# Performance work log

Measured on AMD Instinct MI355X. Metric: run time of the kernel, lower is better.

## Reference

```python
import jax, jax.numpy as jnp
import numpy as np

S = 2048       # seq_len
D = 1024       # d_model
H = 16         # heads
DK = 64        # d_k = d_v = D // H


def setup_inputs() -> dict:
    key = jax.random.key(0)
    ks = jax.random.split(key, 12)
    sc_in = 1.0 / np.sqrt(D)
    return {
        "Q": jax.random.normal(ks[0], (S, D), jnp.float32),
        "K": jax.random.normal(ks[1], (S, D), jnp.float32),
        "V": jax.random.normal(ks[2], (S, D), jnp.float32),
        # stacked per-head projection weights (torch Linear math: x @ W + b, W stored [in,out])
        "Wq": jax.random.normal(ks[3], (H, D, DK), jnp.float32) * sc_in,
        "bq": jnp.zeros((H, DK), jnp.float32),
        "Wk": jax.random.normal(ks[4], (H, D, DK), jnp.float32) * sc_in,
        "bk": jnp.zeros((H, DK), jnp.float32),
        "Wv": jax.random.normal(ks[5], (H, D, DK), jnp.float32) * sc_in,
        "bv": jnp.zeros((H, DK), jnp.float32),
        "Wo": jax.random.normal(ks[6], (H * DK, D), jnp.float32) * (1.0 / np.sqrt(H * DK)),
        "bo": jnp.zeros((D,), jnp.float32),
    }


def reference(Q, K, V, Wq, bq, Wk, bk, Wv, bv, Wo, bo):
    # per-head projections, all heads at once: [S,D] x [H,D,DK] -> [H,S,DK]
    q = jnp.einsum("sd,hdk->hsk", Q, Wq) + bq[:, None, :]
    k = jnp.einsum("sd,hdk->hsk", K, Wk) + bk[:, None, :]
    v = jnp.einsum("sd,hdk->hsk", V, Wv) + bv[:, None, :]
    # scaled dot-product attention per head: [H,S,S]
    scores = jnp.einsum("hsk,htk->hst", q, k) / jnp.sqrt(jnp.asarray(DK, q.dtype))
    attn = jax.nn.softmax(scores, axis=-1)
    heads = jnp.einsum("hst,htv->hsv", attn, v)          # [H,S,DK]
    concat = heads.transpose(1, 0, 2).reshape(S, H * DK)  # [S, H*DK]
    return concat @ Wo + bo                               # [S, D]
```

## Files before the change

kernel.cpp:

```cpp
#include <hip/hip_runtime.h>
#include <stdint.h>

#define S_LEN 2048
#define D_MODEL 1024
#define NH 16
#define DKV 64

typedef unsigned short u16;
typedef __bf16 bf16x8 __attribute__((ext_vector_type(8)));
typedef float f32x4 __attribute__((ext_vector_type(4)));

__device__ __forceinline__ u16 f2bf(float f) {
  union { float f; uint32_t u; } v; v.f = f;
  uint32_t r = v.u + 0x7FFFu + ((v.u >> 16) & 1u);
  return (u16)(r >> 16);
}
__device__ __forceinline__ uint32_t pkbf(float lo, float hi) {
  union { float f; uint32_t u; } a, b; a.f = lo; b.f = hi;
  return ((b.u + 0x8000u) & 0xFFFF0000u) | ((a.u + 0x8000u) >> 16);
}
__device__ __forceinline__ void gl16(const u16* g, u16* l) {
  __builtin_amdgcn_global_load_lds(
      (const __attribute__((address_space(1))) unsigned int*)g,
      (__attribute__((address_space(3))) unsigned int*)l, 16, 0, 0);
}

__global__ __launch_bounds__(256) void prep_k(
    const float* __restrict__ Q, const float* __restrict__ K,
    const float* __restrict__ V, const float* __restrict__ Wq,
    const float* __restrict__ Wk, const float* __restrict__ Wv,
    const float* __restrict__ Wo, u16* __restrict__ QKVb,
    u16* __restrict__ Wqt, u16* __restrict__ Wkt, u16* __restrict__ Wvt,
    u16* __restrict__ Wot) {
  __shared__ float tile[32][33];
  const int idx = blockIdx.x;
  if (idx < 6144) {
    const int z = idx >> 11, blk = idx & 2047;
    const float* src = (z == 0) ? Q : (z == 1) ? K : V;
    u16* dst = QKVb + (size_t)z * S_LEN * D_MODEL;
    size_t i = ((size_t)blk * 256 + threadIdx.x) * 4;
    const float4 v = *(const float4*)(src + i);
    union { u16 h[4]; uint2 u2; } o;
    o.h[0] = f2bf(v.x); o.h[1] = f2bf(v.y); o.h[2] = f2bf(v.z); o.h[3] = f2bf(v.w);
    *(uint2*)(dst + i) = o.u2;
    return;
  }
  const float* ip; u16* op; int R, C, r0, c0;
  if (idx < 9216) {
    int t = idx - 6144;
    int which = t >> 10, head = (t & 1023) >> 6, tl = t & 63;
    ip = ((which == 0) ? Wq : (which == 1) ? Wk : Wv) + (size_t)head * D_MODEL * DKV;
    op = ((which == 0) ? Wqt : (which == 1) ? Wkt : Wvt) + (size_t)head * D_MODEL * DKV;
    R = D_MODEL; C = DKV; c0 = (tl & 1) * 32; r0 = (tl >> 1) * 32;
  } else {
    int t = idx - 9216;
    ip = Wo; op = Wot; R = D_MODEL; C = D_MODEL;
    c0 = (t & 31) * 32; r0 = (t >> 5) * 32;
  }
  int tr = threadIdx.x >> 5, tc = threadIdx.x & 31;
#pragma unroll
  for (int i = 0; i < 4; i++)
    tile[tr + i * 8][tc] = ip[(size_t)(r0 + tr + i * 8) * C + c0 + tc];
  __syncthreads();
#pragma unroll
  for (int i = 0; i < 4; i++) {
    int c = tr + i * 8;
    op[(size_t)(c0 + c) * R + r0 + tc] = f2bf(tile[tc][c]);
  }
}

__global__ __launch_bounds__(256, 2) void proj_gemm_k(
    const u16* __restrict__ qkvb, const u16* __restrict__ Wqt,
    const u16* __restrict__ Wkt, const u16* __restrict__ Wvt,
    const float* __restrict__ bq, const float* __restrict__ bk,
    const float* __restrict__ bv,
    u16* __restrict__ qb, u16* __restrict__ kb, u16* __restrict__ vT) {
  const int bid = blockIdx.x;
  const int l = (bid & 7) * 48 + (bid >> 3);
  const int z = l >> 7, rem = l & 127;
  const int m0 = (rem >> 3) * 128, n0 = (rem & 7) * 128;
  const u16* A = qkvb + (size_t)z * S_LEN * D_MODEL;
  const u16* Bt = (z == 0) ? Wqt : (z == 1) ? Wkt : Wvt;
  const float* bias = (z == 0) ? bq : (z == 1) ? bk : bv;
  const float scale = (z == 0) ? 0.18033688f : 1.0f;

  __shared__ __align__(16) u16 smem[4 * 8192];
  const int tid = threadIdx.x;
  const int w = tid >> 6, lane = tid & 63, quad = lane >> 4, l15 = lane & 15;
  const int wm = (w >> 1) * 64, wn = (w & 1) * 64;
  const int pb = w * 256;

  f32x4 acc[4][4] = {};

  {
    u16* As = smem; u16* Bs = smem + 16384;
#pragma unroll
    for (int e = 0; e < 4; e++) {
      int p = pb + e * 64 + lane;
      int r = p >> 3, cg = (p & 7) ^ (r & 7);
      gl16(&A[(size_t)(m0 + r) * D_MODEL + cg * 8], As + (pb + e * 64) * 8);
      gl16(&Bt[(size_t)(n0 + r) * D_MODEL + cg * 8], Bs + (pb + e * 64) * 8);
    }
  }
  for (int it = 0; it < 16; it++) {
    __syncthreads();
    if (it < 15) {
      const int k0 = (it + 1) * 64;
      u16* As = smem + ((it + 1) & 1) * 8192;
      u16* Bs = smem + 16384 + ((it + 1) & 1) * 8192;
#pragma unroll
      for (int e = 0; e < 4; e++) {
        int p = pb + e * 64 + lane;
        int r = p >> 3, cg = (p & 7) ^ (r & 7);
        gl16(&A[(size_t)(m0 + r) * D_MODEL + k0 + cg * 8], As + (pb + e * 64) * 8);
        gl16(&Bt[(size_t)(n0 + r) * D_MODEL + k0 + cg * 8], Bs + (pb + e * 64) * 8);
      }
    }
    const u16* As = smem + (it & 1) * 8192;
    const u16* Bs = smem + 16384 + (it & 1) * 8192;
#pragma unroll
    for (int kc = 0; kc < 2; kc++) {
      bf16x8 af[4], bfr[4];
      const int c = kc * 4 + quad;
#pragma unroll
      for (int t = 0; t < 4; t++) {
        int ma = wm + t * 16 + l15, na = wn + t * 16 + l15;
        af[t] = *(const bf16x8*)&As[(ma * 8 + (c ^ (ma & 7))) * 8];
        bfr[t] = *(const bf16x8*)&Bs[(na * 8 + (c ^ (na & 7))) * 8];
      }
#pragma unroll
      for (int tm = 0; tm < 4; tm++)
#pragma unroll
        for (int tn = 0; tn < 4; tn++)
          acc[tm][tn] = __builtin_amdgcn_mfma_f32_16x16x32_bf16(af[tm], bfr[tn], acc[tm][tn], 0, 0, 0);
    }
  }

  if (z < 2) {
    u16* O = (z == 0) ? qb : kb;
#pragma unroll
    for (int tm = 0; tm < 4; tm++)
#pragma unroll
      for (int tn = 0; tn < 4; tn++)
#pragma unroll
        for (int r = 0; r < 4; r++) {
          int row = m0 + wm + tm * 16 + quad * 4 + r;
          int col = n0 + wn + tn * 16 + l15;
          O[(size_t)row * D_MODEL + col] = f2bf((acc[tm][tn][r] + bias[col]) * scale);
        }
  } else {
#pragma unroll
    for (int tm = 0; tm < 4; tm++)
#pragma unroll
      for (int tn = 0; tn < 4; tn++) {
        int col = n0 + wn + tn * 16 + l15;
        int row0 = m0 + wm + tm * 16 + quad * 4;
        float b = bias[col];
        union { u16 h[4]; uint2 u2; } o;
#pragma unroll
        for (int r = 0; r < 4; r++) o.h[r] = f2bf(acc[tm][tn][r] + b);
        *(uint2*)&vT[(size_t)col * S_LEN + row0] = o.u2;
      }
  }
}

__global__ __launch_bounds__(512) void attn_k(
    const u16* __restrict__ qb, const u16* __restrict__ kb,
    const u16* __restrict__ vT, u16* __restrict__ conc) {
  const int bid = blockIdx.x;
  const int l = (bid & 7) * 64 + (bid >> 3);
  const int h = l >> 5, qblk = (l & 31) * 64;
  const int tid = threadIdx.x;
  const int w = tid >> 6, lane = tid & 63, quad = lane >> 4, l15 = lane & 15;
  const int half = w >> 2, wq = w & 3;
  const int q0 = qblk + wq * 16;

  __shared__ __align__(16) u16 smem[25600];
  u16* Kh = smem + half * 4096;
  u16* Vh = smem + 8192 + half * 4096;
  u16* Pw = smem + 16384 + w * 1152;

  bf16x8 qf[2];
#pragma unroll
  for (int kc = 0; kc < 2; kc++)
    qf[kc] = *(const bf16x8*)&qb[(size_t)(q0 + l15) * D_MODEL + h * 64 + kc * 32 + quad * 8];

  const u16* kbase = kb + (size_t)h * 64;
  const u16* vbase = vT + (size_t)(h * 64) * S_LEN;

  const int p = wq * 64 + lane;
  const int kr = p >> 3, kcg = (p & 7) ^ (kr & 7);
  const int vr = p >> 2, vcg = (p & 3) ^ (vr & 3);
  const size_t kgoff = (size_t)kr * D_MODEL + kcg * 8;
  const size_t vgoff = (size_t)vr * S_LEN + vcg * 8;
  const int ldsoff = wq * 64 * 8;

  f32x4 oacc[4] = {};
  float lsum = 0.f;

  {
    const int t0 = half * 1024;
    gl16(kbase + (size_t)t0 * D_MODEL + kgoff, Kh + ldsoff);
    gl16(vbase + t0 + vgoff, Vh + ldsoff);
  }

  for (int it = 0; it < 32; it++) {
    __syncthreads();
    if (it < 31) {
      const int t0n = half * 1024 + (it + 1) * 32;
      u16* Kd = Kh + ((it + 1) & 1) * 2048;
      u16* Vd = Vh + ((it + 1) & 1) * 2048;
      gl16(kbase + (size_t)t0n * D_MODEL + kgoff, Kd + ldsoff);
      gl16(vbase + t0n + vgoff, Vd + ldsoff);
    }
    const u16* Kc = Kh + (it & 1) * 2048;
    const u16* Vc = Vh + (it & 1) * 2048;

    f32x4 sacc[2] = {};
#pragma unroll
    for (int kc = 0; kc < 2; kc++)
#pragma unroll
      for (int tn = 0; tn < 2; tn++) {
        int rr = tn * 16 + l15;
        bf16x8 ka = *(const bf16x8*)&Kc[(rr * 8 + ((kc * 4 + quad) ^ (rr & 7))) * 8];
        sacc[tn] = __builtin_amdgcn_mfma_f32_16x16x32_bf16(ka, qf[kc], sacc[tn], 0, 0, 0);
      }

#pragma unroll
    for (int tn = 0; tn < 2; tn++) {
      float p0 = exp2f(sacc[tn][0]);
      float p1 = exp2f(sacc[tn][1]);
      float p2 = exp2f(sacc[tn][2]);
      float p3 = exp2f(sacc[tn][3]);
      lsum += (p0 + p1) + (p2 + p3);
      uint2 pw2; pw2.x = pkbf(p0, p1); pw2.y = pkbf(p2, p3);
      *(uint2*)&Pw[l15 * 72 + tn * 16 + quad * 4] = pw2;
    }

    bf16x8 pa = *(const bf16x8*)&Pw[l15 * 72 + quad * 8];
#pragma unroll
    for (int nt = 0; nt < 4; nt++) {
      int dv = nt * 16 + l15;
      bf16x8 vb = *(const bf16x8*)&Vc[(dv * 4 + (quad ^ (dv & 3))) * 8];
      oacc[nt] = __builtin_amdgcn_mfma_f32_16x16x32_bf16(pa, vb, oacc[nt], 0, 0, 0);
    }
  }
  __syncthreads();

  lsum += __shfl_xor(lsum, 16, 64);
  lsum += __shfl_xor(lsum, 32, 64);

  float* OshF = (float*)smem;
  float* lshF = OshF + 8 * 16 * 68;
  if (lane < 16) lshF[w * 16 + lane] = lsum;
#pragma unroll
  for (int nt = 0; nt < 4; nt++)
#pragma unroll
    for (int r = 0; r < 4; r++)
      OshF[w * 1088 + (quad * 4 + r) * 68 + nt * 16 + l15] = oacc[nt][r];
  __syncthreads();

  const int q = tid >> 3;
  const int dv0 = (tid & 7) * 8;
  const int wa = q >> 4, wb = wa + 4, qr = q & 15;
  const float* pa = &OshF[wa * 1088 + qr * 68 + dv0];
  const float* pb = &OshF[wb * 1088 + qr * 68 + dv0];
  float4 a0 = *(const float4*)pa, a1 = *(const float4*)(pa + 4);
  float4 b0 = *(const float4*)pb, b1 = *(const float4*)(pb + 4);
  float li = 1.0f / (lshF[wa * 16 + qr] + lshF[wb * 16 + qr]);
  union { u16 hh[8]; uint4 u4; } o;
  o.hh[0] = f2bf((a0.x + b0.x) * li); o.hh[1] = f2bf((a0.y + b0.y) * li);
  o.hh[2] = f2bf((a0.z + b0.z) * li); o.hh[3] = f2bf((a0.w + b0.w) * li);
  o.hh[4] = f2bf((a1.x + b1.x) * li); o.hh[5] = f2bf((a1.y + b1.y) * li);
  o.hh[6] = f2bf((a1.z + b1.z) * li); o.hh[7] = f2bf((a1.w + b1.w) * li);
  *(uint4*)&conc[(size_t)(qblk + q) * D_MODEL + h * 64 + dv0] = o.u4;
}

__global__ __launch_bounds__(256, 4) void out_gemm_k(
    const u16* __restrict__ A, const u16* __restrict__ Bt,
    const float* __restrict__ bias, float* __restrict__ out) {
  const int bid = blockIdx.x;
  const int l = (bid & 7) * 64 + (bid >> 3);
  const int m0 = (l >> 4) * 64, n0 = (l & 15) * 64;
  __shared__ __align__(16) u16 smem[4 * 4096];
  const int tid = threadIdx.x;
  const int w = tid >> 6, lane = tid & 63, quad = lane >> 4, l15 = lane & 15;
  const int wm = (w >> 1) * 32, wn = (w & 1) * 32;
  const int pb = w * 128;

  f32x4 acc[2][2] = {};
  {
    u16* As = smem; u16* Bs = smem + 8192;
#pragma unroll
    for (int e = 0; e < 2; e++) {
      int p = pb + e * 64 + lane;
      int r = p >> 3, cg = (p & 7) ^ (r & 7);
      gl16(&A[(size_t)(m0 + r) * D_MODEL + cg * 8], As + (pb + e * 64) * 8);
      gl16(&Bt[(size_t)(n0 + r) * D_MODEL + cg * 8], Bs + (pb + e * 64) * 8);
    }
  }
  for (int it = 0; it < 16; it++) {
    __syncthreads();
    if (it < 15) {
      const int k0 = (it + 1) * 64;
      u16* As = smem + ((it + 1) & 1) * 4096;
      u16* Bs = smem + 8192 + ((it + 1) & 1) * 4096;
#pragma unroll
      for (int e = 0; e < 2; e++) {
        int p = pb + e * 64 + lane;
        int r = p >> 3, cg = (p & 7) ^ (r & 7);
        gl16(&A[(size_t)(m0 + r) * D_MODEL + k0 + cg * 8], As + (pb + e * 64) * 8);
        gl16(&Bt[(size_t)(n0 + r) * D_MODEL + k0 + cg * 8], Bs + (pb + e * 64) * 8);
      }
    }
    const u16* As = smem + (it & 1) * 4096;
    const u16* Bs = smem + 8192 + (it & 1) * 4096;
#pragma unroll
    for (int kc = 0; kc < 2; kc++) {
      const int c = kc * 4 + quad;
      bf16x8 af[2], bfr[2];
#pragma unroll
      for (int t = 0; t < 2; t++) {
        int ma = wm + t * 16 + l15, na = wn + t * 16 + l15;
        af[t] = *(const bf16x8*)&As[(ma * 8 + (c ^ (ma & 7))) * 8];
        bfr[t] = *(const bf16x8*)&Bs[(na * 8 + (c ^ (na & 7))) * 8];
      }
#pragma unroll
      for (int tm = 0; tm < 2; tm++)
#pragma unroll
        for (int tn = 0; tn < 2; tn++)
          acc[tm][tn] = __builtin_amdgcn_mfma_f32_16x16x32_bf16(af[tm], bfr[tn], acc[tm][tn], 0, 0, 0);
    }
  }
#pragma unroll
  for (int tm = 0; tm < 2; tm++)
#pragma unroll
    for (int tn = 0; tn < 2; tn++)
#pragma unroll
      for (int r = 0; r < 4; r++) {
        int row = m0 + wm + tm * 16 + quad * 4 + r;
        int col = n0 + wn + tn * 16 + l15;
        out[(size_t)row * D_MODEL + col] = acc[tm][tn][r] + bias[col];
      }
}

extern "C" void kernel_launch(void* const* d_in, const int* in_sizes, int n_in,
                              void* d_out, int out_size, void* d_ws, size_t ws_size,
                              hipStream_t stream) {
  const float* Q  = (const float*)d_in[0];
  const float* K  = (const float*)d_in[1];
  const float* V  = (const float*)d_in[2];
  const float* Wq = (const float*)d_in[3];
  const float* bq = (const float*)d_in[4];
  const float* Wk = (const float*)d_in[5];
  const float* bk = (const float*)d_in[6];
  const float* Wv = (const float*)d_in[7];
  const float* bv = (const float*)d_in[8];
  const float* Wo = (const float*)d_in[9];
  const float* bo = (const float*)d_in[10];
  float* out = (float*)d_out;

  u16* ws = (u16*)d_ws;
  u16* QKVb = ws;
  u16* Wqt  = QKVb + (size_t)3 * S_LEN * D_MODEL;
  u16* Wkt  = Wqt + (size_t)D_MODEL * D_MODEL;
  u16* Wvt  = Wkt + (size_t)D_MODEL * D_MODEL;
  u16* Wot  = Wvt + (size_t)D_MODEL * D_MODEL;
  u16* qbuf = Wot + (size_t)D_MODEL * D_MODEL;
  u16* kbuf = qbuf + (size_t)S_LEN * D_MODEL;
  u16* vTb  = kbuf + (size_t)S_LEN * D_MODEL;
  u16* conc = vTb + (size_t)S_LEN * D_MODEL;

  prep_k<<<dim3(10240), 256, 0, stream>>>(Q, K, V, Wq, Wk, Wv, Wo,
                                          QKVb, Wqt, Wkt, Wvt, Wot);
  proj_gemm_k<<<dim3(384), 256, 0, stream>>>(
      QKVb, Wqt, Wkt, Wvt, bq, bk, bv, qbuf, kbuf, vTb);
  attn_k<<<dim3(512), 512, 0, stream>>>(qbuf, kbuf, vTb, conc);
  out_gemm_k<<<dim3(512), 256, 0, stream>>>(conc, Wot, bo, out);
}
```

Measured before the change: 165.7 us.

## Triple-buffer K/V and GEMM tiles with explicit vmcnt waits for deeper prefetch

Both the attention kernel and the output GEMM go from double to triple LDS buffering. They issue loads two iterations ahead and replace __syncthreads with an explicit s_waitcnt vmcnt(N) plus s_barrier, so older tile loads can land while newer ones stay in flight. The aim is to hide more global-load latency. The cost is more LDS per block, which lowers occupancy; out_gemm launch bounds drop from 4 to 2 blocks.

```diff
diff --git a/kernel.cpp b/kernel.cpp
--- a/kernel.cpp
+++ b/kernel.cpp
@@ -175,10 +175,10 @@
   const int half = w >> 2, wq = w & 3;
   const int q0 = qblk + wq * 16;
 
-  __shared__ __align__(16) u16 smem[25600];
-  u16* Kh = smem + half * 4096;
-  u16* Vh = smem + 8192 + half * 4096;
-  u16* Pw = smem + 16384 + w * 1152;
+  __shared__ __align__(16) u16 smem[33792];
+  u16* Kh = smem + half * 6144;
+  u16* Vh = smem + 12288 + half * 6144;
+  u16* Pw = smem + 24576 + w * 1152;
 
   bf16x8 qf[2];
 #pragma unroll
@@ -202,19 +202,24 @@
     const int t0 = half * 1024;
     gl16(kbase + (size_t)t0 * D_MODEL + kgoff, Kh + ldsoff);
     gl16(vbase + t0 + vgoff, Vh + ldsoff);
-  }
-
+    const int t1 = t0 + 32;
+    gl16(kbase + (size_t)t1 * D_MODEL + kgoff, Kh + 2048 + ldsoff);
+    gl16(vbase + t1 + vgoff, Vh + 2048 + ldsoff);
+  }
+
+  int rd = 0;
   for (int it = 0; it < 32; it++) {
-    __syncthreads();
-    if (it < 31) {
-      const int t0n = half * 1024 + (it + 1) * 32;
-      u16* Kd = Kh + ((it + 1) & 1) * 2048;
-      u16* Vd = Vh + ((it + 1) & 1) * 2048;
-      gl16(kbase + (size_t)t0n * D_MODEL + kgoff, Kd + ldsoff);
-      gl16(vbase + t0n + vgoff, Vd + ldsoff);
-    }
-    const u16* Kc = Kh + (it & 1) * 2048;
-    const u16* Vc = Vh + (it & 1) * 2048;
+    if (it < 31) asm volatile("s_waitcnt vmcnt(2)" ::: "memory");
+    else         asm volatile("s_waitcnt vmcnt(0)" ::: "memory");
+    __builtin_amdgcn_s_barrier();
+    if (it < 30) {
+      const int wr = (rd == 0) ? 2 : rd - 1;
+      const int t0n = half * 1024 + (it + 2) * 32;
+      gl16(kbase + (size_t)t0n * D_MODEL + kgoff, Kh + wr * 2048 + ldsoff);
+      gl16(vbase + t0n + vgoff, Vh + wr * 2048 + ldsoff);
+    }
+    const u16* Kc = Kh + rd * 2048;
+    const u16* Vc = Vh + rd * 2048;
 
     f32x4 sacc[2] = {};
 #pragma unroll
@@ -244,6 +249,7 @@
       bf16x8 vb = *(const bf16x8*)&Vc[(dv * 4 + (quad ^ (dv & 3))) * 8];
       oacc[nt] = __builtin_amdgcn_mfma_f32_16x16x32_bf16(pa, vb, oacc[nt], 0, 0, 0);
     }
+    rd = (rd == 2) ? 0 : rd + 1;
   }
   __syncthreads();
 
@@ -276,13 +282,13 @@
   *(uint4*)&conc[(size_t)(qblk + q) * D_MODEL + h * 64 + dv0] = o.u4;
 }
 
-__global__ __launch_bounds__(256, 4) void out_gemm_k(
+__global__ __launch_bounds__(256, 2) void out_gemm_k(
     const u16* __restrict__ A, const u16* __restrict__ Bt,
     const float* __restrict__ bias, float* __restrict__ out) {
   const int bid = blockIdx.x;
   const int l = (bid & 7) * 64 + (bid >> 3);
   const int m0 = (l >> 4) * 64, n0 = (l & 15) * 64;
-  __shared__ __align__(16) u16 smem[4 * 4096];
+  __shared__ __align__(16) u16 smem[6 * 4096];
   const int tid = threadIdx.x;
   const int w = tid >> 6, lane = tid & 63, quad = lane >> 4, l15 = lane & 15;
   const int wm = (w >> 1) * 32, wn = (w & 1) * 32;
@@ -290,21 +296,31 @@
 
   f32x4 acc[2][2] = {};
   {
-    u16* As = smem; u16* Bs = smem + 8192;
 #pragma unroll
     for (int e = 0; e < 2; e++) {
       int p = pb + e * 64 + lane;
       int r = p >> 3, cg = (p & 7) ^ (r & 7);
-      gl16(&A[(size_t)(m0 + r) * D_MODEL + cg * 8], As + (pb + e * 64) * 8);
-      gl16(&Bt[(size_t)(n0 + r) * D_MODEL + cg * 8], Bs + (pb + e * 64) * 8);
-    }
-  }
+      gl16(&A[(size_t)(m0 + r) * D_MODEL + cg * 8], smem + (pb + e * 64) * 8);
+      gl16(&Bt[(size_t)(n0 + r) * D_MODEL + cg * 8], smem + 12288 + (pb + e * 64) * 8);
+    }
+#pragma unroll
+    for (int e = 0; e < 2; e++) {
+      int p = pb + e * 64 + lane;
+      int r = p >> 3, cg = (p & 7) ^ (r & 7);
+      gl16(&A[(size_t)(m0 + r) * D_MODEL + 64 + cg * 8], smem + 4096 + (pb + e * 64) * 8);
+      gl16(&Bt[(size_t)(n0 + r) * D_MODEL + 64 + cg * 8], smem + 16384 + (pb + e * 64) * 8);
+    }
+  }
+  int rd = 0;
   for (int it = 0; it < 16; it++) {
-    __syncthreads();
-    if (it < 15) {
-      const int k0 = (it + 1) * 64;
-      u16* As = smem + ((it + 1) & 1) * 4096;
-      u16* Bs = smem + 8192 + ((it + 1) & 1) * 4096;
+    if (it < 15) asm volatile("s_waitcnt vmcnt(4)" ::: "memory");
+    else         asm volatile("s_waitcnt vmcnt(0)" ::: "memory");
+    __builtin_amdgcn_s_barrier();
+    if (it < 14) {
+      const int wr = (rd == 0) ? 2 : rd - 1;
+      const int k0 = (it + 2) * 64;
+      u16* As = smem + wr * 4096;
+      u16* Bs = smem + 12288 + wr * 4096;
 #pragma unroll
       for (int e = 0; e < 2; e++) {
         int p = pb + e * 64 + lane;
@@ -313,8 +329,8 @@
         gl16(&Bt[(size_t)(n0 + r) * D_MODEL + k0 + cg * 8], Bs + (pb + e * 64) * 8);
       }
     }
-    const u16* As = smem + (it & 1) * 4096;
-    const u16* Bs = smem + 8192 + (it & 1) * 4096;
+    const u16* As = smem + rd * 4096;
+    const u16* Bs = smem + 12288 + rd * 4096;
 #pragma unroll
     for (int kc = 0; kc < 2; kc++) {
       const int c = kc * 4 + quad;
@@ -331,6 +347,7 @@
         for (int tn = 0; tn < 2; tn++)
           acc[tm][tn] = __builtin_amdgcn_mfma_f32_16x16x32_bf16(af[tm], bfr[tn], acc[tm][tn], 0, 0, 0);
     }
+    rd = (rd == 2) ? 0 : rd + 1;
   }
 #pragma unroll
   for (int tm = 0; tm < 2; tm++)
```

Result: faster. 160.9 us (-2.9%).
